# Performance work log

Measured on AMD Instinct MI355X. Metric: run time of the kernel, lower is better.

The kernel has to match this reference:

```python
import jax, jax.numpy as jnp
import numpy as np

N = 100000
E = 3200000
IN_DIM = 256
HID = 64
OUT = 40


def setup_inputs() -> dict:
    key = jax.random.key(0)
    ks = jax.random.split(key, 8)
    x = jax.random.normal(ks[0], (N, IN_DIM), dtype=jnp.float32)
    edge_index = jax.random.randint(ks[1], (2, E), 0, N, dtype=jnp.int64)
    # Glorot-ish init for weights
    W1 = jax.random.normal(ks[2], (IN_DIM, HID), dtype=jnp.float32) / np.sqrt(IN_DIM)
    b1 = jnp.zeros((HID,), dtype=jnp.float32)
    W2 = jax.random.normal(ks[3], (HID, HID), dtype=jnp.float32) / np.sqrt(HID)
    b2 = jnp.zeros((HID,), dtype=jnp.float32)
    W3 = jax.random.normal(ks[4], (HID, OUT), dtype=jnp.float32) / np.sqrt(HID)
    b3 = jax.random.normal(ks[5], (OUT,), dtype=jnp.float32) * 0.01
    return {"x": x, "edge_index": edge_index,
            "W1": W1, "b1": b1, "W2": W2, "b2": b2, "W3": W3, "b3": b3}


def _gcn_norm(edge_index, n):
    # Add self-loops, compute symmetric normalization deg^-1/2 A deg^-1/2
    loop = jnp.arange(n, dtype=edge_index.dtype)
    src = jnp.concatenate([edge_index[0], loop])
    dst = jnp.concatenate([edge_index[1], loop])
    deg = jax.ops.segment_sum(jnp.ones_like(dst, dtype=jnp.float32), dst,
                              num_segments=n)
    dinv = jnp.where(deg > 0, jax.lax.rsqrt(deg), 0.0)
    norm = dinv[src] * dinv[dst]  # [E+N]
    return src, dst, norm


def _gcn_conv(x, src, dst, norm, W, b, n):
    h = x @ W                                  # transform first (small dim)
    msg = h[src] * norm[:, None]               # gather + scale
    out = jax.ops.segment_sum(msg, dst, num_segments=n)  # scatter-add
    return out + b


def reference(x, edge_index, W1, b1, W2, b2, W3, b3):
    n = x.shape[0]
    src, dst, norm = _gcn_norm(edge_index, n)
    h = jax.nn.relu(_gcn_conv(x, src, dst, norm, W1, b1, n))
    h = jax.nn.relu(_gcn_conv(h, src, dst, norm, W2, b2, n))
    logits = h @ W3 + b3
    return jax.nn.log_softmax(logits, axis=1)
```

## Files before the change

### kernel.cpp

```cpp
#include <hip/hip_runtime.h>
#include <hip/hip_fp16.h>
#include <cstdint>


constexpr int CHUNK = 8192;
constexpr int BKCAP = 8192;

typedef __attribute__((ext_vector_type(8))) short bf16x8;
typedef __attribute__((ext_vector_type(4))) float f32x4;

__device__ __forceinline__ int cvt2bf(float a, float b) {
    int r;
    asm volatile("v_cvt_pk_bf16_f32 %0, %1, %2" : "=v"(r) : "v"(a), "v"(b));
    return r;
}

__global__ __launch_bounds__(256) void p2_localsort(
        const int* __restrict__ esrc, const int* __restrict__ edst, int E,
        unsigned* __restrict__ pairs1, int* __restrict__ cntMat,
        int* __restrict__ startMat, int NBK) {
    __shared__ int hist[1024];
    __shared__ int wsum[256];
    __shared__ unsigned lp[CHUNK];
    const int t = threadIdx.x, blk = blockIdx.x;
    const int base = blk * CHUNK;
    const int cnt = min(CHUNK, E - base);
    for (int i = t; i < 1024; i += 256) hist[i] = 0;
    __syncthreads();
    for (int i = t; i < cnt; i += 256) atomicAdd(&hist[edst[base + i] >> 7], 1);
    __syncthreads();
    int h0 = hist[4*t], h1 = hist[4*t+1], h2 = hist[4*t+2], h3 = hist[4*t+3];
    int s = h0 + h1 + h2 + h3;
    wsum[t] = s; __syncthreads();
    #pragma unroll
    for (int o = 1; o < 256; o <<= 1) {
        int x = (t >= o) ? wsum[t - o] : 0;
        __syncthreads(); wsum[t] += x; __syncthreads();
    }
    int run = wsum[t] - s;
    int e0 = run, e1 = run + h0, e2 = e1 + h1, e3 = e2 + h2;
    hist[4*t] = e0; hist[4*t+1] = e1; hist[4*t+2] = e2; hist[4*t+3] = e3;
    if (4*t     < NBK) { cntMat[(size_t)blk*NBK + 4*t]     = h0; startMat[(size_t)blk*NBK + 4*t]     = e0; }
    if (4*t + 1 < NBK) { cntMat[(size_t)blk*NBK + 4*t + 1] = h1; startMat[(size_t)blk*NBK + 4*t + 1] = e1; }
    if (4*t + 2 < NBK) { cntMat[(size_t)blk*NBK + 4*t + 2] = h2; startMat[(size_t)blk*NBK + 4*t + 2] = e2; }
    if (4*t + 3 < NBK) { cntMat[(size_t)blk*NBK + 4*t + 3] = h3; startMat[(size_t)blk*NBK + 4*t + 3] = e3; }
    __syncthreads();
    for (int i = t; i < cnt; i += 256) {
        int d = edst[base + i];
        int pos = atomicAdd(&hist[d >> 7], 1);
        lp[pos] = ((unsigned)(d & 127) << 17) | (unsigned)esrc[base + i];
    }
    __syncthreads();
    for (int i = t; i < cnt; i += 256) pairs1[base + i] = lp[i];
}

__global__ __launch_bounds__(256) void p3_colscan(int* __restrict__ cntMat,
        int* __restrict__ TB, int nchunks, int NBK) {
    __shared__ int buf[512];
    const int t = threadIdx.x, b = blockIdx.x;
    int v0 = (t < nchunks) ? cntMat[(size_t)t*NBK + b] : 0;
    int v1 = (t + 256 < nchunks) ? cntMat[(size_t)(t + 256)*NBK + b] : 0;
    buf[t] = v0; buf[t + 256] = v1; __syncthreads();
    #pragma unroll
    for (int o = 1; o < 512; o <<= 1) {
        int x0 = (t >= o) ? buf[t - o] : 0;
        int x1 = (t + 256 >= o) ? buf[t + 256 - o] : 0;
        __syncthreads(); buf[t] += x0; buf[t + 256] += x1; __syncthreads();
    }
    if (t < nchunks) cntMat[(size_t)t*NBK + b] = buf[t] - v0;
    if (t + 256 < nchunks) cntMat[(size_t)(t + 256)*NBK + b] = buf[t + 256] - v1;
    if (t == 0) TB[b] = buf[511];
}

__global__ __launch_bounds__(256) void p4_scan(const int* __restrict__ TB,
        int* __restrict__ bucketBase, int NBK, int E) {
    __shared__ int buf[1024];
    __shared__ int wsum[256];
    const int t = threadIdx.x;
    for (int i = t; i < 1024; i += 256) buf[i] = (i < NBK) ? TB[i] : 0;
    __syncthreads();
    int h0 = buf[4*t], h1 = buf[4*t+1], h2 = buf[4*t+2], h3 = buf[4*t+3];
    int s = h0 + h1 + h2 + h3;
    wsum[t] = s; __syncthreads();
    #pragma unroll
    for (int o = 1; o < 256; o <<= 1) {
        int x = (t >= o) ? wsum[t - o] : 0;
        __syncthreads(); wsum[t] += x; __syncthreads();
    }
    int run = wsum[t] - s;
    int e0 = run, e1 = run + h0, e2 = e1 + h1, e3 = e2 + h2;
    if (4*t     < NBK) bucketBase[4*t]     = e0;
    if (4*t + 1 < NBK) bucketBase[4*t + 1] = e1;
    if (4*t + 2 < NBK) bucketBase[4*t + 2] = e2;
    if (4*t + 3 < NBK) bucketBase[4*t + 3] = e3;
    if (t == 0) bucketBase[NBK] = E;
}

__global__ __launch_bounds__(256) void p6_sortcsr(
        const unsigned* __restrict__ pairs1, const int* __restrict__ cumMat,
        const int* __restrict__ startMat, const int* __restrict__ TB,
        const int* __restrict__ bucketBase, int nchunks, int NBK,
        int* __restrict__ csrc, int* __restrict__ rofs,
        float* __restrict__ dinv, int N, int E) {
    __shared__ unsigned lp[BKCAP];
    __shared__ int ccum[512];
    __shared__ int cstart[512];
    __shared__ int hist[128];
    __shared__ int sc[128];
    __shared__ int foffs[128];
    const int t = threadIdx.x, b = blockIdx.x;
    const int total0 = TB[b];
    const int total = min(total0, BKCAP);
    const int base = bucketBase[b];
    for (int i = t; i < nchunks; i += 256) {
        ccum[i]   = cumMat[(size_t)i * NBK + b];
        cstart[i] = startMat[(size_t)i * NBK + b];
    }
    if (t < 128) hist[t] = 0;
    if (t == 0) ccum[nchunks] = total0;
    __syncthreads();
    for (int i = t; i < total; i += 256) {
        int lo = 0, hi = nchunks - 1;
        while (lo < hi) {
            int mid = (lo + hi + 1) >> 1;
            if (ccum[mid] <= i) lo = mid; else hi = mid - 1;
        }
        unsigned v = pairs1[(size_t)lo * CHUNK + cstart[lo] + (i - ccum[lo])];
        lp[i] = v;
        atomicAdd(&hist[v >> 17], 1);
    }
    __syncthreads();
    if (t < 128) sc[t] = hist[t];
    __syncthreads();
    #pragma unroll
    for (int o = 1; o < 128; o <<= 1) {
        int x = (t >= o && t < 128) ? sc[t - o] : 0;
        __syncthreads();
        if (t < 128) sc[t] += x;
        __syncthreads();
    }
    if (t < 128) {
        int excl = sc[t] - hist[t];
        foffs[t] = excl;
        int node = b * 128 + t;
        if (node < N) {
            rofs[node] = base + excl;
            dinv[node] = rsqrtf((float)hist[t] + 1.0f);
        }
    }
    if (b == 0 && t == 255) rofs[N] = E;
    __syncthreads();
    for (int i = t; i < total; i += 256) {
        unsigned v = lp[i];
        int pos = atomicAdd(&foffs[v >> 17], 1);
        csrc[base + pos] = (int)(v & 0x1FFFFu);
    }
}

template<int K>
__global__ __launch_bounds__(256) void k_gemm(const float* __restrict__ X,
        const float* __restrict__ Wm, const float* __restrict__ dinv,
        __half* __restrict__ G, int nrows) {
    constexpr int KP = K + 8;
    __shared__ unsigned short Wt[64 * KP];
    const int t = threadIdx.x;
    for (int i = t; i < K * 64; i += 256) {
        int k = i >> 6, n = i & 63;
        Wt[n * KP + k] = (unsigned short)(cvt2bf(Wm[i], Wm[i]) & 0xFFFF);
    }
    __syncthreads();
    const int l  = t & 63;
    const int c16 = l & 15;
    const int g4  = l >> 4;
    const int wglob  = blockIdx.x * 4 + (t >> 6);
    const int nwaves = gridDim.x * 4;
    const int ntiles = nrows >> 4;

    for (int tile = wglob; tile < ntiles; tile += nwaves) {
        const int rbase = tile * 16;
        f32x4 acc[4] = {{0,0,0,0},{0,0,0,0},{0,0,0,0},{0,0,0,0}};
        const float* xrow = X + (size_t)(rbase + c16) * K + g4 * 8;
        #pragma unroll
        for (int kc = 0; kc < K / 32; ++kc) {
            float4 u = *(const float4*)(xrow + kc * 32);
            float4 v = *(const float4*)(xrow + kc * 32 + 4);
            int4 ap;
            ap.x = cvt2bf(u.x, u.y); ap.y = cvt2bf(u.z, u.w);
            ap.z = cvt2bf(v.x, v.y); ap.w = cvt2bf(v.z, v.w);
            bf16x8 a = *(bf16x8*)&ap;
            #pragma unroll
            for (int cg = 0; cg < 4; ++cg) {
                bf16x8 bb = *(bf16x8*)(&Wt[(cg * 16 + c16) * KP + kc * 32 + g4 * 8]);
                acc[cg] = __builtin_amdgcn_mfma_f32_16x16x32_bf16(a, bb, acc[cg], 0, 0, 0);
            }
        }
        #pragma unroll
        for (int r = 0; r < 4; ++r) {
            int grow = rbase + g4 * 4 + r;
            float dv = dinv[grow];
            #pragma unroll
            for (int cg = 0; cg < 4; ++cg)
                G[(size_t)grow * 64 + cg * 16 + c16] = __float2half(acc[cg][r] * dv);
        }
    }
}

#define ACC8H(HA, V) { \
    HA[0] = __hadd2(HA[0], *(const __half2*)&(V).x); \
    HA[1] = __hadd2(HA[1], *(const __half2*)&(V).y); \
    HA[2] = __hadd2(HA[2], *(const __half2*)&(V).z); \
    HA[3] = __hadd2(HA[3], *(const __half2*)&(V).w); }

__global__ __launch_bounds__(256) void k_agg(const __half* __restrict__ G,
        const int* __restrict__ rofs, const int* __restrict__ csrc,
        const float* __restrict__ dinv, const float* __restrict__ bias,
        float* __restrict__ H, int nrows) {
    const int l = threadIdx.x & 63;
    const int g = l >> 3;
    const int p = l & 7;
    const int d = blockIdx.x * 4 + (threadIdx.x >> 6);
    if (d >= nrows) return;
    const int beg = rofs[d], end = rofs[d + 1];
    __half2 ha[4];
    #pragma unroll
    for (int q = 0; q < 4; ++q) ha[q] = __half2(__float2half(0.f), __float2half(0.f));

    int e = beg + g;
    for (; e + 8 < end; e += 16) {
        int s0 = csrc[e];
        int s1 = csrc[e + 8];
        uint4 v0 = *(const uint4*)(G + (size_t)s0 * 64 + p * 8);
        uint4 v1 = *(const uint4*)(G + (size_t)s1 * 64 + p * 8);
        ACC8H(ha, v0)
        ACC8H(ha, v1)
    }
    if (e < end) {
        int s = csrc[e];
        uint4 v = *(const uint4*)(G + (size_t)s * 64 + p * 8);
        ACC8H(ha, v)
    }
    #pragma unroll
    for (int off = 8; off <= 32; off <<= 1) {
        #pragma unroll
        for (int q = 0; q < 4; ++q) {
            int o = __shfl_xor(*(int*)&ha[q], off);
            ha[q] = __hadd2(ha[q], *(__half2*)&o);
        }
    }
    if (g == 0) {
        float2 a0 = __half22float2(ha[0]), a1 = __half22float2(ha[1]);
        float2 a2 = __half22float2(ha[2]), a3 = __half22float2(ha[3]);
        uint4 sv = *(const uint4*)(G + (size_t)d * 64 + p * 8);
        float2 s0 = __half22float2(*(const __half2*)&sv.x);
        float2 s1 = __half22float2(*(const __half2*)&sv.y);
        float2 s2 = __half22float2(*(const __half2*)&sv.z);
        float2 s3 = __half22float2(*(const __half2*)&sv.w);
        const float dv = dinv[d];
        const float4* B4 = (const float4*)bias;
        float4 b0 = B4[p * 2], b1 = B4[p * 2 + 1];
        float4 o0, o1;
        o0.x = fmaxf((a0.x + s0.x) * dv + b0.x, 0.f);
        o0.y = fmaxf((a0.y + s0.y) * dv + b0.y, 0.f);
        o0.z = fmaxf((a1.x + s1.x) * dv + b0.z, 0.f);
        o0.w = fmaxf((a1.y + s1.y) * dv + b0.w, 0.f);
        o1.x = fmaxf((a2.x + s2.x) * dv + b1.x, 0.f);
        o1.y = fmaxf((a2.y + s2.y) * dv + b1.y, 0.f);
        o1.z = fmaxf((a3.x + s3.x) * dv + b1.z, 0.f);
        o1.w = fmaxf((a3.y + s3.y) * dv + b1.w, 0.f);
        float4* H4 = (float4*)(H + (size_t)d * 64 + p * 8);
        H4[0] = o0; H4[1] = o1;
    }
}

__global__ __launch_bounds__(256) void k_final(const float* __restrict__ H,
        const float* __restrict__ W3, const float* __restrict__ b3,
        float* __restrict__ out, int nrows) {
    constexpr int HP = 68;
    constexpr int OP = 44;
    __shared__ float wl[64 * 40];
    __shared__ float bl[40];
    __shared__ float Hs[256 * HP];
    const int t = threadIdx.x;
    for (int i = t; i < 640; i += 256)
        ((float4*)wl)[i] = ((const float4*)W3)[i];
    if (t < 40) bl[t] = b3[t];
    const int brow = blockIdx.x * 256;
    const int rows = min(256, nrows - brow);
    for (int i = t; i < rows * 16; i += 256) {
        int r = i >> 4, c = i & 15;
        float4 v = ((const float4*)(H + (size_t)(brow + r) * 64))[c];
        *(float4*)&Hs[r * HP + c * 4] = v;
    }
    __syncthreads();

    float acc[40];
    float lse = 0.f;
    if (t < rows) {
        #pragma unroll
        for (int j = 0; j < 40; ++j) acc[j] = bl[j];
        #pragma unroll
        for (int k4 = 0; k4 < 16; ++k4) {
            float4 h4 = *(const float4*)&Hs[t * HP + k4 * 4];
            float hv[4] = {h4.x, h4.y, h4.z, h4.w};
            #pragma unroll
            for (int c = 0; c < 4; ++c) {
                const float4* wr = (const float4*)(wl + (k4 * 4 + c) * 40);
                #pragma unroll
                for (int j4 = 0; j4 < 10; ++j4) {
                    float4 wv = wr[j4];
                    acc[j4 * 4 + 0] += hv[c] * wv.x;
                    acc[j4 * 4 + 1] += hv[c] * wv.y;
                    acc[j4 * 4 + 2] += hv[c] * wv.z;
                    acc[j4 * 4 + 3] += hv[c] * wv.w;
                }
            }
        }
        float m = acc[0];
        #pragma unroll
        for (int j = 1; j < 40; ++j) m = fmaxf(m, acc[j]);
        float s = 0.f;
        #pragma unroll
        for (int j = 0; j < 40; ++j) s += expf(acc[j] - m);
        lse = m + logf(s);
    }
    __syncthreads();
    float* Os = Hs;
    if (t < rows) {
        #pragma unroll
        for (int j4 = 0; j4 < 10; ++j4)
            *(float4*)&Os[t * OP + j4 * 4] =
                make_float4(acc[j4 * 4 + 0] - lse, acc[j4 * 4 + 1] - lse,
                            acc[j4 * 4 + 2] - lse, acc[j4 * 4 + 3] - lse);
    }
    __syncthreads();
    for (int i = t; i < rows * 40; i += 256) {
        int r = i / 40, c = i - r * 40;
        out[(size_t)brow * 40 + i] = Os[r * OP + c];
    }
}

extern "C" void kernel_launch(void* const* d_in, const int* in_sizes, int n_in,
                              void* d_out, int out_size, void* d_ws, size_t ws_size,
                              hipStream_t stream) {
    const float* x  = (const float*)d_in[0];
    const int*   ei = (const int*)d_in[1];
    const float* W1 = (const float*)d_in[2];
    const float* b1 = (const float*)d_in[3];
    const float* W2 = (const float*)d_in[4];
    const float* b2 = (const float*)d_in[5];
    const float* W3 = (const float*)d_in[6];
    const float* b3 = (const float*)d_in[7];
    float* out = (float*)d_out;

    const int HID = in_sizes[3];
    const int IND = in_sizes[2] / HID;
    const int N   = in_sizes[0] / IND;
    const int E   = in_sizes[1] / 2;
    (void)HID; (void)n_in; (void)out_size; (void)ws_size;

    const int NBK     = (N + 127) >> 7;
    const int nchunks = (E + CHUNK - 1) / CHUNK;

    char* ws = (char*)d_ws;
    size_t off = 0;
    auto alloc = [&](size_t bytes) -> char* {
        char* p = ws + off;
        off = (off + bytes + 255) & ~(size_t)255;
        return p;
    };
    size_t gbytes = (size_t)N * 64 * 2;
    size_t p1bytes = (size_t)E * 4;
    int*      cntMat     = (int*)     alloc((size_t)nchunks * NBK * 4);
    int*      startMat   = (int*)     alloc((size_t)nchunks * NBK * 4);
    int*      TB         = (int*)     alloc((size_t)NBK * 4);
    int*      bucketBase = (int*)     alloc(((size_t)NBK + 1) * 4);
    float*    dinv       = (float*)   alloc((size_t)N * 4);
    int*      rofs       = (int*)     alloc(((size_t)N + 1) * 4);
    int*      csrc       = (int*)     alloc((size_t)E * 4);
    __half*   g          = (__half*)  alloc(gbytes > p1bytes ? gbytes : p1bytes);
    float*    h          = (float*)   alloc((size_t)N * 64 * 4);
    unsigned* pairs1     = (unsigned*)g;

    const int* esrc = ei;
    const int* edst = ei + E;
    const int gG = 782;
    const int gN = (N + 255) / 256;

    p2_localsort<<<nchunks, 256, 0, stream>>>(esrc, edst, E, pairs1, cntMat, startMat, NBK);
    p3_colscan  <<<NBK, 256, 0, stream>>>(cntMat, TB, nchunks, NBK);
    p4_scan     <<<1, 256, 0, stream>>>(TB, bucketBase, NBK, E);
    p6_sortcsr  <<<NBK, 256, 0, stream>>>(pairs1, cntMat, startMat, TB, bucketBase,
                                          nchunks, NBK, csrc, rofs, dinv, N, E);

    k_gemm<256> <<<gG, 256, 0, stream>>>(x, W1, dinv, g, N);
    k_agg       <<<(N + 3) / 4, 256, 0, stream>>>(g, rofs, csrc, dinv, b1, h, N);
    k_gemm<64>  <<<gG, 256, 0, stream>>>(h, W2, dinv, g, N);
    k_agg       <<<(N + 3) / 4, 256, 0, stream>>>(g, rofs, csrc, dinv, b2, h, N);
    k_final     <<<gN, 256, 0, stream>>>(h, W3, b3, out, N);
}
```

Baseline: 270.2 us.

## Stage GEMM X tiles through swizzled shared memory with double-buffered prefetch

The GEMM kernel now gives each block one 64-row tile instead of grid-striding 16-row tiles per wave. X chunks are loaded cooperatively with coalesced float4 reads into an XOR-swizzled, double-buffered shared array, with register prefetch of the next chunk. Output rows are staged through shared memory so each row goes out as wide uint4 stores instead of scattered 2-byte writes. This targets uncoalesced global reads and writes, at the cost of many more blocks, extra shared memory, and a barrier per K chunk.

```diff
diff --git a/kernel.cpp b/kernel.cpp
--- a/kernel.cpp
+++ b/kernel.cpp
@@ -11,7 +11,7 @@
 
 __device__ __forceinline__ int cvt2bf(float a, float b) {
     int r;
-    asm volatile("v_cvt_pk_bf16_f32 %0, %1, %2" : "=v"(r) : "v"(a), "v"(b));
+    asm("v_cvt_pk_bf16_f32 %0, %1, %2" : "=v"(r) : "v"(a), "v"(b));
     return r;
 }
 
@@ -161,47 +161,86 @@
 __global__ __launch_bounds__(256) void k_gemm(const float* __restrict__ X,
         const float* __restrict__ Wm, const float* __restrict__ dinv,
         __half* __restrict__ G, int nrows) {
-    constexpr int KP = K + 8;
+    constexpr int KP  = K + 4;
+    constexpr int NCH = K / 32;
     __shared__ unsigned short Wt[64 * KP];
+    __shared__ float Xs[2][64 * 32];
     const int t = threadIdx.x;
     for (int i = t; i < K * 64; i += 256) {
         int k = i >> 6, n = i & 63;
         Wt[n * KP + k] = (unsigned short)(cvt2bf(Wm[i], Wm[i]) & 0xFFFF);
     }
-    __syncthreads();
-    const int l  = t & 63;
+    const int l   = t & 63;
+    const int w   = t >> 6;
     const int c16 = l & 15;
     const int g4  = l >> 4;
-    const int wglob  = blockIdx.x * 4 + (t >> 6);
-    const int nwaves = gridDim.x * 4;
-    const int ntiles = nrows >> 4;
-
-    for (int tile = wglob; tile < ntiles; tile += nwaves) {
-        const int rbase = tile * 16;
-        f32x4 acc[4] = {{0,0,0,0},{0,0,0,0},{0,0,0,0},{0,0,0,0}};
-        const float* xrow = X + (size_t)(rbase + c16) * K + g4 * 8;
-        #pragma unroll
-        for (int kc = 0; kc < K / 32; ++kc) {
-            float4 u = *(const float4*)(xrow + kc * 32);
-            float4 v = *(const float4*)(xrow + kc * 32 + 4);
-            int4 ap;
-            ap.x = cvt2bf(u.x, u.y); ap.y = cvt2bf(u.z, u.w);
-            ap.z = cvt2bf(v.x, v.y); ap.w = cvt2bf(v.z, v.w);
-            bf16x8 a = *(bf16x8*)&ap;
-            #pragma unroll
-            for (int cg = 0; cg < 4; ++cg) {
-                bf16x8 bb = *(bf16x8*)(&Wt[(cg * 16 + c16) * KP + kc * 32 + g4 * 8]);
-                acc[cg] = __builtin_amdgcn_mfma_f32_16x16x32_bf16(a, bb, acc[cg], 0, 0, 0);
+    const int brow = blockIdx.x * 64;
+
+    int srcoff[2], dstoff[2];
+    #pragma unroll
+    for (int i = 0; i < 2; ++i) {
+        int s = t + i * 256;
+        int row = s >> 3, ks = s & 7;
+        int gr = min(brow + row, nrows - 1);
+        srcoff[i] = gr * K + ks * 4;
+        dstoff[i] = row * 32 + ((ks ^ (row & 7)) << 2);
+    }
+
+    float4 r0 = *(const float4*)(X + (size_t)srcoff[0]);
+    float4 r1 = *(const float4*)(X + (size_t)srcoff[1]);
+    *(float4*)(&Xs[0][dstoff[0]]) = r0;
+    *(float4*)(&Xs[0][dstoff[1]]) = r1;
+    if (NCH > 1) {
+        r0 = *(const float4*)(X + (size_t)srcoff[0] + 32);
+        r1 = *(const float4*)(X + (size_t)srcoff[1] + 32);
+    }
+    __syncthreads();
+
+    f32x4 acc[4] = {{0,0,0,0},{0,0,0,0},{0,0,0,0},{0,0,0,0}};
+    const int xrow = (w * 16 + c16) * 32;
+    const int xsw  = (w * 16 + c16) & 7;
+
+    for (int ch = 0; ch < NCH; ++ch) {
+        if (ch + 1 < NCH) {
+            *(float4*)(&Xs[(ch + 1) & 1][dstoff[0]]) = r0;
+            *(float4*)(&Xs[(ch + 1) & 1][dstoff[1]]) = r1;
+            if (ch + 2 < NCH) {
+                r0 = *(const float4*)(X + (size_t)srcoff[0] + (ch + 2) * 32);
+                r1 = *(const float4*)(X + (size_t)srcoff[1] + (ch + 2) * 32);
             }
         }
-        #pragma unroll
-        for (int r = 0; r < 4; ++r) {
-            int grow = rbase + g4 * 4 + r;
-            float dv = dinv[grow];
-            #pragma unroll
-            for (int cg = 0; cg < 4; ++cg)
-                G[(size_t)grow * 64 + cg * 16 + c16] = __float2half(acc[cg][r] * dv);
-        }
+        const float* xb = Xs[ch & 1];
+        float4 u = *(const float4*)(xb + xrow + (((g4 * 2 + 0) ^ xsw) << 2));
+        float4 v = *(const float4*)(xb + xrow + (((g4 * 2 + 1) ^ xsw) << 2));
+        int4 ap;
+        ap.x = cvt2bf(u.x, u.y); ap.y = cvt2bf(u.z, u.w);
+        ap.z = cvt2bf(v.x, v.y); ap.w = cvt2bf(v.z, v.w);
+        bf16x8 a = *(bf16x8*)&ap;
+        #pragma unroll
+        for (int cg = 0; cg < 4; ++cg) {
+            bf16x8 bb = *(bf16x8*)(&Wt[(cg * 16 + c16) * KP + ch * 32 + g4 * 8]);
+            acc[cg] = __builtin_amdgcn_mfma_f32_16x16x32_bf16(a, bb, acc[cg], 0, 0, 0);
+        }
+        __syncthreads();
+    }
+
+    __half* scr = (__half*)(&Xs[0][0]) + w * (16 * 72);
+    #pragma unroll
+    for (int r = 0; r < 4; ++r) {
+        int grow = brow + w * 16 + g4 * 4 + r;
+        float dv = (grow < nrows) ? dinv[grow] : 0.f;
+        #pragma unroll
+        for (int cg = 0; cg < 4; ++cg)
+            scr[(g4 * 4 + r) * 72 + cg * 16 + c16] = __float2half(acc[cg][r] * dv);
+    }
+    __syncthreads();
+    const int row16 = l >> 2, q = l & 3;
+    const int grow = brow + w * 16 + row16;
+    uint4 d0 = *(const uint4*)(scr + row16 * 72 + q * 16);
+    uint4 d1 = *(const uint4*)(scr + row16 * 72 + q * 16 + 8);
+    if (grow < nrows) {
+        *(uint4*)(G + (size_t)grow * 64 + q * 16)     = d0;
+        *(uint4*)(G + (size_t)grow * 64 + q * 16 + 8) = d1;
     }
 }
 
@@ -383,7 +422,7 @@
 
     const int* esrc = ei;
     const int* edst = ei + E;
-    const int gG = 782;
+    const int gM = (N + 63) / 64;
     const int gN = (N + 255) / 256;
 
     p2_localsort<<<nchunks, 256, 0, stream>>>(esrc, edst, E, pairs1, cntMat, startMat, NBK);
@@ -392,9 +431,9 @@
     p6_sortcsr  <<<NBK, 256, 0, stream>>>(pairs1, cntMat, startMat, TB, bucketBase,
                                           nchunks, NBK, csrc, rofs, dinv, N, E);
 
-    k_gemm<256> <<<gG, 256, 0, stream>>>(x, W1, dinv, g, N);
+    k_gemm<256> <<<gM, 256, 0, stream>>>(x, W1, dinv, g, N);
     k_agg       <<<(N + 3) / 4, 256, 0, stream>>>(g, rofs, csrc, dinv, b1, h, N);
-    k_gemm<64>  <<<gG, 256, 0, stream>>>(h, W2, dinv, g, N);
+    k_gemm<64>  <<<gM, 256, 0, stream>>>(h, W2, dinv, g, N);
     k_agg       <<<(N + 3) / 4, 256, 0, stream>>>(g, rofs, csrc, dinv, b2, h, N);
     k_final     <<<gN, 256, 0, stream>>>(h, W3, b3, out, N);
 }
```

New measurement: 302.8 us. +12.1%, slower.
